# Optimization experiments

Measured on AMD Instinct MI355X. Metric: run time of the kernel, lower is better.

The kernel has to match this reference:

```python
import jax, jax.numpy as jnp
from jax import lax
import numpy as np

DIM = 768      # model dim
NL = 12        # num mamba layers
DS = 16        # d_state
DI = 1536      # d_inner = 2*dim
DC = 4         # d_conv
P = 16         # patch size
IMG = 256
NP = (IMG // P) ** 2  # 256 patches
GS = 5         # KAN grid_size
SO = 3         # KAN spline_order
NK = NL // 3   # 4 KAN layers
BATCH = 32


def setup_inputs() -> dict:
    key = jax.random.key(0)
    ks = jax.random.split(key, 16)
    def n(k, shape, s=0.02):
        return jax.random.normal(k, shape, jnp.float32) * s
    return {
        "x": jax.random.normal(ks[0], (BATCH, 3, IMG, IMG), jnp.float32),
        "patch_w": n(ks[1], (DIM, 3, P, P)),
        "patch_b": jnp.zeros((DIM,), jnp.float32),
        "pos_embed": n(ks[2], (1, NP, DIM)),
        "in_proj_w": n(ks[3], (NL, 2 * DI, DIM)),
        "conv_w": n(ks[4], (NL, DI, 1, DC), 0.1),
        "conv_b": jnp.zeros((NL, DI), jnp.float32),
        "x_proj_w": n(ks[5], (NL, 2 * DS, DI)),
        "dt_proj_w": n(ks[6], (NL, DS, DI)),
        "dt_proj_b": jnp.zeros((NL, DS), jnp.float32),
        "A_log": jnp.tile(jnp.log(jnp.arange(1, DS + 1, dtype=jnp.float32)), (NL, 1)),
        "D_param": jnp.ones((NL, DI), jnp.float32),
        "out_proj_w": n(ks[7], (NL, DIM, DI)),
        "kan_base_w": n(ks[8], (NK, DIM, DIM)),
        "kan_coeff": n(ks[9], (NK, DIM, DIM, GS + SO), 0.1),
        "kan_bias": n(ks[10], (NK, DIM), 0.01),
        "norm_w": jnp.ones((DIM,), jnp.float32),
        "norm_b": jnp.zeros((DIM,), jnp.float32),
    }


def _mamba_block(x, in_w, cw, cb, xpw, dtw, dtb, alog, Dp, ow):
    Bsz, L, _ = x.shape
    xr = jnp.einsum('bld,ed->ble', x, in_w)              # [B,L,2*DI]
    x1, res = xr[..., :DI], xr[..., DI:]
    # causal depthwise conv (pad d_conv-1 on left, truncate to L)
    xc = lax.conv_general_dilated(
        x1.transpose(0, 2, 1), cw, (1,), [(DC - 1, 0)],
        feature_group_count=DI,
        dimension_numbers=('NCH', 'OIH', 'NCH')) + cb[None, :, None]
    x1 = jax.nn.silu(xc.transpose(0, 2, 1))              # [B,L,DI]
    x_dbl = jnp.einsum('bld,ed->ble', x1, xpw)           # [B,L,2*DS]
    Bp = x_dbl[..., DS:]                                 # dt half of x_proj is discarded (as in torch)
    dt = jax.nn.softplus(jnp.einsum('bld,nd->bln', x1, dtw) + dtb)  # [B,L,DS]
    A = -jnp.exp(alog)                                   # [DS]
    Ad = jnp.exp(A * dt)                                 # [B,L,DS]
    u = x1[..., :DI // DS].mean(-1)                      # [B,L]
    Bd = dt * Bp * u[..., None]                          # [B,L,DS]
    def step(s, ab):
        a, b = ab
        s = s * a + b
        return s, s
    _, ys = lax.scan(step, jnp.zeros((Bsz, DS), x.dtype),
                     (Ad.transpose(1, 0, 2), Bd.transpose(1, 0, 2)))
    y = ys.transpose(1, 0, 2)                            # [B,L,DS]
    y = jnp.repeat(y, DI // DS, axis=-1)                 # n -> (n d)
    y = y + x1 * Dp
    y = y * jax.nn.silu(res)
    return jnp.einsum('bld,ed->ble', y, ow)              # [B,L,DIM]


def _kan(xf, bw, coeff, bias):
    base = xf @ bw.T + bias
    grid = jnp.linspace(-1.0, 1.0, GS + 1)
    denom = grid[1:] - grid[:-1] + 1e-8
    xs = (xf[..., None] - grid[:-1]) / denom             # [M,DIM,GS]
    basis = jnp.where((xs >= 0) & (xs < 1), xs, 0.0)
    return base + jnp.einsum('bik,oik->bo', basis, coeff[:, :, :GS])


def reference(x, patch_w, patch_b, pos_embed, in_proj_w, conv_w, conv_b,
              x_proj_w, dt_proj_w, dt_proj_b, A_log, D_param, out_proj_w,
              kan_base_w, kan_coeff, kan_bias, norm_w, norm_b):
    Bsz = x.shape[0]
    h = lax.conv_general_dilated(
        x, patch_w, (P, P), 'VALID',
        dimension_numbers=('NCHW', 'OIHW', 'NCHW')) + patch_b[None, :, None, None]
    h = h.transpose(0, 2, 3, 1).reshape(Bsz, NP, DIM) + pos_embed
    for i in range(NL):
        h = _mamba_block(h, in_proj_w[i], conv_w[i], conv_b[i], x_proj_w[i],
                         dt_proj_w[i], dt_proj_b[i], A_log[i], D_param[i], out_proj_w[i])
        if i % 3 == 2 and i // 3 < NK:
            j = i // 3
            hf = h.reshape(-1, DIM)
            h = _kan(hf, kan_base_w[j], kan_coeff[j], kan_bias[j]).reshape(Bsz, NP, DIM) + h
    mu = h.mean(-1, keepdims=True)
    var = ((h - mu) ** 2).mean(-1, keepdims=True)
    return (h - mu) / jnp.sqrt(var + 1e-5) * norm_w + norm_b
```

## Files before the change

### kernel.cpp

```cpp
#include <hip/hip_runtime.h>

#define BATCH 32
#define NPATCH 256
#define MROWS (BATCH * NPATCH)
#define DIM 768
#define DI 1536
#define DS 16

typedef __bf16 bf16_t;
typedef __attribute__((ext_vector_type(8))) __bf16 bf16x8;
typedef __attribute__((ext_vector_type(4))) float floatx4;

__device__ __forceinline__ float bf2f(unsigned short u) {
    union { unsigned int i; float f; } v; v.i = ((unsigned int)u) << 16; return v.f;
}
__device__ __forceinline__ unsigned short f2bf(float f) {
    union { float f; unsigned int i; } u; u.f = f;
    unsigned int r = u.i + 0x7FFFu + ((u.i >> 16) & 1u);
    return (unsigned short)(r >> 16);
}
__device__ __forceinline__ float ldin(const void* p, int i, int bf) {
    if (bf) return bf2f(((const unsigned short*)p)[i]);
    return ((const float*)p)[i];
}
__device__ __forceinline__ float4 ldin4(const void* p, int i, int bf) {
    if (bf) {
        ushort4 u = *(const ushort4*)((const unsigned short*)p + i);
        return make_float4(bf2f(u.x), bf2f(u.y), bf2f(u.z), bf2f(u.w));
    }
    return *(const float4*)((const float*)p + i);
}
__device__ __forceinline__ float siluf(float x) { return x / (1.0f + expf(-x)); }

__global__ void detect_k(const void* alog, int* flag) {
    if (threadIdx.x == 0 && blockIdx.x == 0) {
        float v = ((const float*)alog)[1];
        flag[0] = (fabsf(v - 0.69314718f) < 0.01f) ? 0 : 1;
    }
}

__global__ __launch_bounds__(256) void cvt4_k(const int* __restrict__ flag,
                                              const void* __restrict__ in,
                                              unsigned short* __restrict__ out, int n4) {
    int i = blockIdx.x * 256 + threadIdx.x;
    if (i >= n4) return;
    float4 v = ldin4(in, i * 4, flag[0]);
    ushort4 o;
    o.x = f2bf(v.x); o.y = f2bf(v.y); o.z = f2bf(v.z); o.w = f2bf(v.w);
    *(ushort4*)(out + i * 4) = o;
}

__global__ __launch_bounds__(256) void kcoef_k(const int* __restrict__ flag,
                                               const void* __restrict__ co,
                                               bf16_t* __restrict__ out) {
    int idx = blockIdx.x * 256 + threadIdx.x;
    int bf = flag[0];
    int j = idx / (768 * 3840);
    int r = idx - j * (768 * 3840);
    int n = r / 3840;
    int kk = r - n * 3840;
    int i = kk / 5, k5 = kk - i * 5;
    out[idx] = (bf16_t)ldin(co, ((j * 768 + n) * 768 + i) * 8 + k5, bf);
}

__global__ __launch_bounds__(256) void wproj_k(const int* __restrict__ flag,
                                               const void* __restrict__ dtw,
                                               const void* __restrict__ xpw,
                                               bf16_t* __restrict__ w2) {
    int idx = blockIdx.x * 256 + threadIdx.x;
    int bf = flag[0];
    int i = idx / (128 * 1536);
    int r = idx - i * (128 * 1536);
    int n = r / 1536, k = r - n * 1536;
    float v;
    if (n < 16)       v = ldin(dtw, (i * 16 + n) * 1536 + k, bf);
    else if (n < 32)  v = ldin(xpw, (i * 32 + n) * 1536 + k, bf);
    else if (n == 32) v = (k < 96) ? (1.0f / 96.0f) : 0.0f;
    else              v = 0.0f;
    w2[idx] = (bf16_t)v;
}

__global__ __launch_bounds__(256) void cvtconv_k(const int* __restrict__ flag,
                                                 const void* __restrict__ cw,
                                                 bf16_t* __restrict__ cwr) {
    int idx = blockIdx.x * 256 + threadIdx.x;
    int bf = flag[0];
    int i = idx / (4 * 1536);
    int r = idx - i * (4 * 1536);
    int k = r / 1536, c = r - k * 1536;
    cwr[idx] = (bf16_t)ldin(cw, i * 1536 * 4 + c * 4 + k, bf);
}

__global__ __launch_bounds__(256) void basis_k(const bf16_t* __restrict__ h,
                                               bf16_t* __restrict__ bas) {
    int idx = blockIdx.x * 256 + threadIdx.x;
    int m = idx / 96, i8 = (idx - m * 96) * 8;
    bf16x8 hv = *(const bf16x8*)(h + (size_t)m * 768 + i8);
    union { bf16_t a[40]; bf16x8 v[5]; } ob;
#pragma unroll
    for (int ii = 0; ii < 8; ii++) {
        float xv = (float)hv[ii];
#pragma unroll
        for (int k5 = 0; k5 < 5; k5++) {
            float tt = (xv + 1.0f - 0.4f * (float)k5) * 2.5f;
            ob.a[ii * 5 + k5] = (bf16_t)((tt >= 0.0f && tt < 1.0f) ? tt : 0.0f);
        }
    }
    bf16_t* op = bas + (size_t)m * 3840 + (size_t)i8 * 5;
#pragma unroll
    for (int j = 0; j < 5; j++) *(bf16x8*)(op + j * 8) = ob.v[j];
}

__global__ __launch_bounds__(256) void im2col_k(const int* __restrict__ flag,
                                                const void* __restrict__ x,
                                                bf16_t* __restrict__ xp) {
    int idx = blockIdx.x * 256 + threadIdx.x;
    int bf = flag[0];
    int m = idx / 768, kc = idx - m * 768;
    int b = m >> 8, p = m & 255;
    int py = p >> 4, px = p & 15;
    int c = kc >> 8, rr = kc & 255;
    int ky = rr >> 4, kx = rr & 15;
    int src = ((b * 3 + c) * 256 + py * 16 + ky) * 256 + px * 16 + kx;
    xp[idx] = (bf16_t)ldin(x, src, bf);
}

__global__ __launch_bounds__(256) void mgemm_k(
    const bf16_t* __restrict__ A, int lda,
    const bf16_t* __restrict__ W, int ldw,
    bf16_t* __restrict__ C, int ldc,
    int K, int mode, int gx,
    const int* __restrict__ flag,
    const void* __restrict__ bias, int boff,
    const void* __restrict__ aux, int aoff,
    const bf16_t* __restrict__ H, int ldh,
    float* __restrict__ dtu) {
    __shared__ bf16_t sm[2][2 * 128 * 64];
    const int t = threadIdx.x;
    const int lane = t & 63, wave = t >> 6;
    const int wm = wave >> 1, wn = wave & 1;

    int m0, n0, kbeg, kend;
    if (mode == 5) {
        int mt = blockIdx.x >> 2, ks = blockIdx.x & 3;
        m0 = mt << 7; n0 = 0;
        int KS = K >> 2;
        kbeg = ks * KS; kend = kbeg + KS;
    } else {
        const int bid = blockIdx.x;
        const int xcd = bid & 7, l = bid >> 3;
        const int w = gx < 8 ? gx : 8;
        const int cb8 = w * 8;
        const int ch = l / cb8, rem = l - ch * cb8;
        const int mi = rem / w, ni = rem - mi * w;
        m0 = (xcd * 8 + mi) << 7;
        n0 = (ch * w + ni) << 7;
        kbeg = 0; kend = K;
    }

    const int srow = t >> 3;
    const int colperm = (((t & 7) ^ (srow & 7)) << 3);
    const bf16_t* gA[4]; const bf16_t* gB[4];
#pragma unroll
    for (int r = 0; r < 4; r++) {
        gA[r] = A + (size_t)(m0 + r * 32 + srow) * lda + colperm;
        gB[r] = W + (size_t)(n0 + r * 32 + srow) * ldw + colperm;
    }

    floatx4 acc[4][4];
#pragma unroll
    for (int i = 0; i < 4; i++)
#pragma unroll
        for (int j = 0; j < 4; j++) acc[i][j] = (floatx4){0.f, 0.f, 0.f, 0.f};

    const int kq = lane >> 4;
    const int mr = lane & 15;

    auto stage = [&](int buf, int kt) {
        char* sa = (char*)&sm[buf][0];
#pragma unroll
        for (int r = 0; r < 4; r++) {
            const int off = r * 4096 + wave * 1024;
            __builtin_amdgcn_global_load_lds(
                (const __attribute__((address_space(1))) unsigned int*)(gA[r] + kt),
                (__attribute__((address_space(3))) unsigned int*)(sa + off), 16, 0, 0);
            __builtin_amdgcn_global_load_lds(
                (const __attribute__((address_space(1))) unsigned int*)(gB[r] + kt),
                (__attribute__((address_space(3))) unsigned int*)(sa + 16384 + off), 16, 0, 0);
        }
    };

    auto compute = [&](int buf) {
        const bf16_t* sAc = &sm[buf][0];
        const bf16_t* sBc = sAc + 128 * 64;
#pragma unroll
        for (int half = 0; half < 2; half++) {
            const int cb = half * 4 + kq;
            if (mode == 5) {
                if (wn == 0) {
                    bf16x8 af[4], bw3[3];
#pragma unroll
                    for (int i = 0; i < 4; i++) {
                        int rw = wm * 64 + i * 16 + mr;
                        af[i] = *(const bf16x8*)(sAc + rw * 64 + ((cb ^ (rw & 7)) << 3));
                    }
#pragma unroll
                    for (int j = 0; j < 3; j++) {
                        int rw = j * 16 + mr;
                        bw3[j] = *(const bf16x8*)(sBc + rw * 64 + ((cb ^ (rw & 7)) << 3));
                    }
#pragma unroll
                    for (int i = 0; i < 4; i++)
#pragma unroll
                        for (int j = 0; j < 3; j++)
                            acc[i][j] = __builtin_amdgcn_mfma_f32_16x16x32_bf16(af[i], bw3[j], acc[i][j], 0, 0, 0);
                }
            } else {
                bf16x8 af[4], bw[4];
#pragma unroll
                for (int i = 0; i < 4; i++) {
                    int rw = wm * 64 + i * 16 + mr;
                    af[i] = *(const bf16x8*)(sAc + rw * 64 + ((cb ^ (rw & 7)) << 3));
                }
#pragma unroll
                for (int j = 0; j < 4; j++) {
                    int rw = wn * 64 + j * 16 + mr;
                    bw[j] = *(const bf16x8*)(sBc + rw * 64 + ((cb ^ (rw & 7)) << 3));
                }
#pragma unroll
                for (int i = 0; i < 4; i++)
#pragma unroll
                    for (int j = 0; j < 4; j++)
                        acc[i][j] = __builtin_amdgcn_mfma_f32_16x16x32_bf16(af[i], bw[j], acc[i][j], 0, 0, 0);
            }
        }
    };

    stage(0, kbeg);
    int cur = 0;
    for (int kt = kbeg; kt < kend; kt += 64) {
        if (kt + 64 < kend) {
            stage(cur ^ 1, kt + 64);
            asm volatile("s_waitcnt vmcnt(8)" ::: "memory");
        } else {
            asm volatile("s_waitcnt vmcnt(0)" ::: "memory");
        }
        asm volatile("s_barrier" ::: "memory");
        compute(cur);
        asm volatile("s_barrier" ::: "memory");
        cur ^= 1;
    }

    const int col = lane & 15;
    const int rq = (lane >> 4) * 4;

    if (mode == 5) {
        if (wn == 0) {
            int ks = blockIdx.x & 3;
            float* dst = dtu + (size_t)ks * (MROWS * 64);
#pragma unroll
            for (int i = 0; i < 4; i++) {
#pragma unroll
                for (int reg = 0; reg < 4; reg++) {
                    int gm = m0 + wm * 64 + i * 16 + rq + reg;
#pragma unroll
                    for (int j = 0; j < 3; j++) {
                        int gn = j * 16 + col;
                        if (gn <= 32)
                            dst[(size_t)gm * 64 + gn] = acc[i][j][reg];
                    }
                }
            }
        }
        return;
    }

    const int bff = (mode == 1 || mode == 2) ? flag[0] : 0;
#pragma unroll
    for (int i = 0; i < 4; i++) {
#pragma unroll
        for (int reg = 0; reg < 4; reg++) {
            int gm = m0 + wm * 64 + i * 16 + rq + reg;
#pragma unroll
            for (int j = 0; j < 4; j++) {
                int gn = n0 + wn * 64 + j * 16 + col;
                float v = acc[i][j][reg];
                if (mode == 1) v += ldin(bias, boff + gn, bff) + ldin(aux, aoff + (gm & 255) * 768 + gn, bff);
                else if (mode == 2) v += ldin(bias, boff + gn, bff);
                else if (mode == 3) v += (float)C[(size_t)gm * ldc + gn] + (float)H[(size_t)gm * ldh + gn];
                C[(size_t)gm * ldc + gn] = (bf16_t)v;
            }
        }
    }
}

__global__ __launch_bounds__(256) void conv_k(const int* __restrict__ flag,
                                              const bf16_t* __restrict__ xr,
                                              const bf16_t* __restrict__ cwr,
                                              const void* __restrict__ cb, int cbo,
                                              bf16_t* __restrict__ xc) {
    int idx = blockIdx.x * 256 + threadIdx.x;
    int bf = flag[0];
    int m = idx / 192, c8 = (idx - m * 192) * 8;
    int l = m & 255;
    float acc[8];
    float4 b0 = ldin4(cb, cbo + c8, bf), b1 = ldin4(cb, cbo + c8 + 4, bf);
    acc[0] = b0.x; acc[1] = b0.y; acc[2] = b0.z; acc[3] = b0.w;
    acc[4] = b1.x; acc[5] = b1.y; acc[6] = b1.z; acc[7] = b1.w;
#pragma unroll
    for (int k = 0; k < 4; k++) {
        if (l + k - 3 >= 0) {
            bf16x8 xv = *(const bf16x8*)(xr + (size_t)(m + k - 3) * 3072 + c8);
            bf16x8 wv = *(const bf16x8*)(cwr + k * 1536 + c8);
#pragma unroll
            for (int j = 0; j < 8; j++) acc[j] += (float)xv[j] * (float)wv[j];
        }
    }
    bf16x8 o;
#pragma unroll
    for (int j = 0; j < 8; j++) o[j] = (bf16_t)siluf(acc[j]);
    *(bf16x8*)(xc + (size_t)m * 1536 + c8) = o;
}

__global__ __launch_bounds__(256) void scan_k(const int* __restrict__ flag,
                                              const float* __restrict__ dtu,
                                              const void* __restrict__ dtb, int dtbo,
                                              const void* __restrict__ alog, int alo,
                                              float* __restrict__ ys) {
    int wid = (blockIdx.x * 256 + threadIdx.x) >> 6;
    int lane = threadIdx.x & 63;
    int b = wid >> 4, s = wid & 15;
    int bf = flag[0];
    float dtbv = ldin(dtb, dtbo + s, bf);
    float Av = -expf(ldin(alog, alo + s, bf));
    const float* pb = dtu + (size_t)b * (256 * 64);
    float* yo = ys + (size_t)b * (256 * 16);
    float Aj[4], Bj[4];
    float A = 1.0f, Bv = 0.0f;
#pragma unroll
    for (int j = 0; j < 4; j++) {
        int l = lane * 4 + j;
        float rdt = dtbv, rBp = 0.0f, ru = 0.0f;
#pragma unroll
        for (int ks = 0; ks < 4; ks++) {
            const float* q = pb + (size_t)ks * (MROWS * 64) + (size_t)l * 64;
            rdt += q[s];
            rBp += q[16 + s];
            ru  += q[32];
        }
        float dt = (rdt > 20.0f) ? rdt : log1pf(expf(rdt));
        float a = expf(Av * dt);
        float bb = dt * rBp * ru;
        Bv = Bv * a + bb;
        A = A * a;
        Aj[j] = A; Bj[j] = Bv;
    }
#pragma unroll
    for (int off = 1; off < 64; off <<= 1) {
        float pa = __shfl_up(A, off);
        float pb2 = __shfl_up(Bv, off);
        if (lane >= off) { Bv = pb2 * A + Bv; A = pa * A; }
    }
    float ex = __shfl_up(Bv, 1);
    if (lane == 0) ex = 0.0f;
#pragma unroll
    for (int j = 0; j < 4; j++) {
        int l = lane * 4 + j;
        yo[l * 16 + s] = Aj[j] * ex + Bj[j];
    }
}

__global__ __launch_bounds__(256) void gate_k(const int* __restrict__ flag,
                                              const float* __restrict__ ys,
                                              bf16_t* __restrict__ xc,
                                              const bf16_t* __restrict__ xr,
                                              const void* __restrict__ Dp, int dpo) {
    int idx = blockIdx.x * 256 + threadIdx.x;
    int bf = flag[0];
    int m = idx / 192, d8 = (idx - m * 192) * 8;
    float yv = ys[m * 16 + d8 / 96];
    bf16x8 rv = *(const bf16x8*)(xr + (size_t)m * 3072 + 1536 + d8);
    bf16x8 xv = *(const bf16x8*)(xc + (size_t)m * 1536 + d8);
    float4 dp0 = ldin4(Dp, dpo + d8, bf), dp1 = ldin4(Dp, dpo + d8 + 4, bf);
    float dpv[8] = {dp0.x, dp0.y, dp0.z, dp0.w, dp1.x, dp1.y, dp1.z, dp1.w};
    bf16x8 o;
#pragma unroll
    for (int j = 0; j < 8; j++) {
        float v = yv + (float)xv[j] * dpv[j];
        o[j] = (bf16_t)(v * siluf((float)rv[j]));
    }
    *(bf16x8*)(xc + (size_t)m * 1536 + d8) = o;
}

__global__ __launch_bounds__(256) void lnorm_k(const int* __restrict__ flag,
                                               const bf16_t* __restrict__ h,
                                               const void* __restrict__ nw,
                                               const void* __restrict__ nb,
                                               void* __restrict__ out) {
    __shared__ float ls[4];
    int bf = flag[0];
    int m = blockIdx.x, t = threadIdx.x;
    const bf16_t* row = h + (size_t)m * 768;
    float v0 = (float)row[t], v1 = (float)row[t + 256], v2 = (float)row[t + 512];
    float s = v0 + v1 + v2;
#pragma unroll
    for (int o = 32; o; o >>= 1) s += __shfl_xor(s, o);
    if ((t & 63) == 0) ls[t >> 6] = s;
    __syncthreads();
    float mu = (ls[0] + ls[1] + ls[2] + ls[3]) * (1.0f / 768.0f);
    __syncthreads();
    float d0 = v0 - mu, d1 = v1 - mu, d2 = v2 - mu;
    float q = d0 * d0 + d1 * d1 + d2 * d2;
#pragma unroll
    for (int o = 32; o; o >>= 1) q += __shfl_xor(q, o);
    if ((t & 63) == 0) ls[t >> 6] = q;
    __syncthreads();
    float var = (ls[0] + ls[1] + ls[2] + ls[3]) * (1.0f / 768.0f);
    float inv = rsqrtf(var + 1e-5f);
    float vv[3] = {d0, d1, d2};
#pragma unroll
    for (int j = 0; j < 3; j++) {
        int colx = t + 256 * j;
        float o = vv[j] * inv * ldin(nw, colx, bf) + ldin(nb, colx, bf);
        size_t oi = (size_t)m * 768 + colx;
        if (bf) ((unsigned short*)out)[oi] = f2bf(o);
        else    ((float*)out)[oi] = o;
    }
}

extern "C" void kernel_launch(void* const* d_in, const int* in_sizes, int n_in,
                              void* d_out, int out_size, void* d_ws, size_t ws_size,
                              hipStream_t stream) {
    const void* x        = d_in[0];
    const void* patch_w  = d_in[1];
    const void* patch_b  = d_in[2];
    const void* pos      = d_in[3];
    const void* in_w     = d_in[4];
    const void* conv_w   = d_in[5];
    const void* conv_b   = d_in[6];
    const void* xpw      = d_in[7];
    const void* dtw      = d_in[8];
    const void* dtb      = d_in[9];
    const void* alog     = d_in[10];
    const void* Dp       = d_in[11];
    const void* out_w    = d_in[12];
    const void* kbw      = d_in[13];
    const void* kcoef    = d_in[14];
    const void* kbias    = d_in[15];
    const void* nw       = d_in[16];
    const void* nb       = d_in[17];

    char* base = (char*)d_ws;
    size_t off = 0;
    int* flag = (int*)base;                          off += 256;
    float* dtu  = (float*)(base + off);              off += (size_t)4 * MROWS * 64 * 4;
    float* ysb  = (float*)(base + off);              off += (size_t)MROWS * 16 * 4;
    bf16_t* hA  = (bf16_t*)(base + off);             off += (size_t)MROWS * DIM * 2;
    bf16_t* hB  = (bf16_t*)(base + off);             off += (size_t)MROWS * DIM * 2;
    bf16_t* xr  = (bf16_t*)(base + off);             off += (size_t)MROWS * 2 * DI * 2;
    bf16_t* xc  = (bf16_t*)(base + off);             off += (size_t)MROWS * DI * 2;
    bf16_t* wpatch = (bf16_t*)(base + off);          off += (size_t)DIM * DIM * 2;
    bf16_t* win  = (bf16_t*)(base + off);            off += (size_t)12 * 2 * DI * DIM * 2;
    bf16_t* wout = (bf16_t*)(base + off);            off += (size_t)12 * DIM * DI * 2;
    bf16_t* wkbw = (bf16_t*)(base + off);            off += (size_t)4 * DIM * DIM * 2;
    bf16_t* wkco = (bf16_t*)(base + off);            off += (size_t)4 * DIM * 3840 * 2;
    bf16_t* w2   = (bf16_t*)(base + off);            off += (size_t)12 * 128 * DI * 2;
    bf16_t* cwr  = (bf16_t*)(base + off);            off += (size_t)12 * 4 * DI * 2;
    bf16_t* basis = xr;
    bf16_t* im2c  = xr;

    detect_k<<<1, 64, 0, stream>>>(alog, flag);

    cvt4_k<<<(DIM * DIM / 4 + 255) / 256, 256, 0, stream>>>(flag, patch_w, (unsigned short*)wpatch, DIM * DIM / 4);
    cvt4_k<<<(12 * 2 * DI * DIM / 4 + 255) / 256, 256, 0, stream>>>(flag, in_w, (unsigned short*)win, 12 * 2 * DI * DIM / 4);
    cvt4_k<<<(12 * DIM * DI / 4 + 255) / 256, 256, 0, stream>>>(flag, out_w, (unsigned short*)wout, 12 * DIM * DI / 4);
    cvt4_k<<<(4 * DIM * DIM / 4 + 255) / 256, 256, 0, stream>>>(flag, kbw, (unsigned short*)wkbw, 4 * DIM * DIM / 4);
    kcoef_k<<<4 * DIM * 3840 / 256, 256, 0, stream>>>(flag, kcoef, wkco);
    wproj_k<<<12 * 128 * DI / 256, 256, 0, stream>>>(flag, dtw, xpw, w2);
    cvtconv_k<<<12 * 4 * DI / 256, 256, 0, stream>>>(flag, conv_w, cwr);

    im2col_k<<<(MROWS * DIM) / 256, 256, 0, stream>>>(flag, x, im2c);
    mgemm_k<<<6 * 64, 256, 0, stream>>>(
        im2c, DIM, wpatch, DIM, hA, DIM, DIM, 1, 6,
        flag, patch_b, 0, pos, 0, nullptr, 0, nullptr);

    bf16_t* hcur = hA;
    bf16_t* hoth = hB;
    for (int i = 0; i < 12; i++) {
        mgemm_k<<<24 * 64, 256, 0, stream>>>(
            hcur, DIM, win + (size_t)i * 2 * DI * DIM, DIM, xr, 2 * DI, DIM, 0, 24,
            flag, nullptr, 0, nullptr, 0, nullptr, 0, nullptr);
        conv_k<<<(MROWS * 192) / 256, 256, 0, stream>>>(
            flag, xr, cwr + (size_t)i * 4 * DI, conv_b, i * DI, xc);
        mgemm_k<<<256, 256, 0, stream>>>(
            xc, DI, w2 + (size_t)i * 128 * DI, DI, nullptr, 128, DI, 5, 1,
            flag, nullptr, 0, nullptr, 0, nullptr, 0, dtu);
        scan_k<<<128, 256, 0, stream>>>(flag, dtu, dtb, i * DS, alog, i * DS, ysb);
        gate_k<<<(MROWS * 192) / 256, 256, 0, stream>>>(
            flag, ysb, xc, xr, Dp, i * DI);
        mgemm_k<<<6 * 64, 256, 0, stream>>>(
            xc, DI, wout + (size_t)i * DIM * DI, DI, hcur, DIM, DI, 0, 6,
            flag, nullptr, 0, nullptr, 0, nullptr, 0, nullptr);
        if (i % 3 == 2) {
            int j = i / 3;
            mgemm_k<<<6 * 64, 256, 0, stream>>>(
                hcur, DIM, wkbw + (size_t)j * DIM * DIM, DIM, hoth, DIM, DIM, 2, 6,
                flag, kbias, j * DIM, nullptr, 0, nullptr, 0, nullptr);
            basis_k<<<(MROWS * 96) / 256, 256, 0, stream>>>(hcur, basis);
            mgemm_k<<<6 * 64, 256, 0, stream>>>(
                basis, 3840, wkco + (size_t)j * DIM * 3840, 3840, hoth, DIM, 3840, 3, 6,
                flag, nullptr, 0, nullptr, 0, hcur, DIM, nullptr);
            bf16_t* tmp = hcur; hcur = hoth; hoth = tmp;
        }
    }

    lnorm_k<<<MROWS, 256, 0, stream>>>(flag, hcur, nw, nb, d_out);
}
```

Baseline: 2.591 ms.

## Use 256x256-tile GEMM kernel with direct global-to-LDS loads for in_proj

```diff
diff --git a/kernel.cpp b/kernel.cpp
--- a/kernel.cpp
+++ b/kernel.cpp
@@ -289,6 +289,109 @@
                 else if (mode == 2) v += ldin(bias, boff + gn, bff);
                 else if (mode == 3) v += (float)C[(size_t)gm * ldc + gn] + (float)H[(size_t)gm * ldh + gn];
                 C[(size_t)gm * ldc + gn] = (bf16_t)v;
+            }
+        }
+    }
+}
+
+__global__ __launch_bounds__(512, 2) void mgemm256_k(
+    const bf16_t* __restrict__ A, int lda,
+    const bf16_t* __restrict__ W, int ldw,
+    bf16_t* __restrict__ C, int ldc,
+    int K) {
+    __shared__ bf16_t sm[2][2 * 256 * 64];
+    const int t = threadIdx.x;
+    const int lane = t & 63, wave = t >> 6;
+    const int wm = wave >> 2, wn = wave & 3;
+
+    const int bid = blockIdx.x;
+    const int xcd = bid & 7, l = bid >> 3;
+    const int mi = l & 3, ni = l >> 2;
+    const int m0 = (xcd * 4 + mi) << 8;
+    const int n0 = ni << 8;
+
+    const int srow = t >> 3;
+    const int colperm = (((t & 7) ^ (srow & 7)) << 3);
+    const bf16_t* gA[4]; const bf16_t* gB[4];
+#pragma unroll
+    for (int r = 0; r < 4; r++) {
+        gA[r] = A + (size_t)(m0 + r * 64 + srow) * lda + colperm;
+        gB[r] = W + (size_t)(n0 + r * 64 + srow) * ldw + colperm;
+    }
+
+    floatx4 acc[8][4];
+#pragma unroll
+    for (int i = 0; i < 8; i++)
+#pragma unroll
+        for (int j = 0; j < 4; j++) acc[i][j] = (floatx4){0.f, 0.f, 0.f, 0.f};
+
+    const int kq = lane >> 4;
+    const int mr = lane & 15;
+
+    auto stage = [&](int buf, int kt) {
+        char* sa = (char*)&sm[buf][0];
+#pragma unroll
+        for (int r = 0; r < 4; r++) {
+            const int off = (r * 512 + t) * 16;
+            __builtin_amdgcn_global_load_lds(
+                (const __attribute__((address_space(1))) unsigned int*)(gA[r] + kt),
+                (__attribute__((address_space(3))) unsigned int*)(sa + off), 16, 0, 0);
+            __builtin_amdgcn_global_load_lds(
+                (const __attribute__((address_space(1))) unsigned int*)(gB[r] + kt),
+                (__attribute__((address_space(3))) unsigned int*)(sa + 32768 + off), 16, 0, 0);
+        }
+    };
+
+    stage(0, 0);
+    int cur = 0;
+    for (int kt = 0; kt < K; kt += 64) {
+        asm volatile("s_waitcnt vmcnt(0)" ::: "memory");
+        asm volatile("s_barrier" ::: "memory");
+        if (kt + 64 < K) stage(cur ^ 1, kt + 64);
+        const bf16_t* sAc = &sm[cur][0];
+        const bf16_t* sBc = sAc + 256 * 64;
+#pragma unroll
+        for (int half = 0; half < 2; half++) {
+            const int cb = half * 4 + kq;
+            bf16x8 bw[4];
+#pragma unroll
+            for (int j = 0; j < 4; j++) {
+                int rw = wn * 64 + j * 16 + mr;
+                bw[j] = *(const bf16x8*)(sBc + rw * 64 + ((cb ^ (rw & 7)) << 3));
+            }
+#pragma unroll
+            for (int ib = 0; ib < 2; ib++) {
+                bf16x8 af[4];
+#pragma unroll
+                for (int i2 = 0; i2 < 4; i2++) {
+                    int rw = wm * 128 + (ib * 4 + i2) * 16 + mr;
+                    af[i2] = *(const bf16x8*)(sAc + rw * 64 + ((cb ^ (rw & 7)) << 3));
+                }
+                __builtin_amdgcn_s_setprio(1);
+#pragma unroll
+                for (int i2 = 0; i2 < 4; i2++)
+#pragma unroll
+                    for (int j = 0; j < 4; j++)
+                        acc[ib * 4 + i2][j] = __builtin_amdgcn_mfma_f32_16x16x32_bf16(
+                            af[i2], bw[j], acc[ib * 4 + i2][j], 0, 0, 0);
+                __builtin_amdgcn_s_setprio(0);
+                asm volatile("s_barrier" ::: "memory");
+            }
+        }
+        cur ^= 1;
+    }
+
+    const int col = lane & 15;
+    const int rq = (lane >> 4) * 4;
+#pragma unroll
+    for (int i = 0; i < 8; i++) {
+#pragma unroll
+        for (int reg = 0; reg < 4; reg++) {
+            int gm = m0 + wm * 128 + i * 16 + rq + reg;
+#pragma unroll
+            for (int j = 0; j < 4; j++) {
+                int gn = n0 + wn * 64 + j * 16 + col;
+                C[(size_t)gm * ldc + gn] = (bf16_t)acc[i][j][reg];
             }
         }
     }
@@ -487,9 +590,8 @@
     bf16_t* hcur = hA;
     bf16_t* hoth = hB;
     for (int i = 0; i < 12; i++) {
-        mgemm_k<<<24 * 64, 256, 0, stream>>>(
-            hcur, DIM, win + (size_t)i * 2 * DI * DIM, DIM, xr, 2 * DI, DIM, 0, 24,
-            flag, nullptr, 0, nullptr, 0, nullptr, 0, nullptr);
+        mgemm256_k<<<384, 512, 0, stream>>>(
+            hcur, DIM, win + (size_t)i * 2 * DI * DIM, DIM, xr, 2 * DI, DIM);
         conv_k<<<(MROWS * 192) / 256, 256, 0, stream>>>(
             flag, xr, cwr + (size_t)i * 4 * DI, conv_b, i * DI, xc);
         mgemm_k<<<256, 256, 0, stream>>>(
```

After: 2.592 ms. Within noise of the previous version (+0.0%).
